# Kernel optimization log

Measured on AMD Instinct MI355X. Metric: run time of the kernel, lower is better.

Reference implementation:

```python
import jax, jax.numpy as jnp
import numpy as np
import math

EMBED_DIM = 1024
NUM_HEADS = 16
QK_DIM = 64
SCALE = 1.0 / math.sqrt(QK_DIM)  # beta=None -> 1/sqrt(qk_dim)


def setup_inputs() -> dict:
    key = jax.random.key(0)
    k1, k2, k3 = jax.random.split(key, 3)
    hidden_states = jax.random.normal(k1, (2, 2048, EMBED_DIM), dtype=jnp.float32)
    # nn.init.normal_(std=0.002)
    query_proj = 0.002 * jax.random.normal(k2, (NUM_HEADS, QK_DIM, EMBED_DIM), dtype=jnp.float32)
    key_proj = 0.002 * jax.random.normal(k3, (NUM_HEADS, QK_DIM, EMBED_DIM), dtype=jnp.float32)
    query_bias = jnp.zeros((QK_DIM,), dtype=jnp.float32)
    key_bias = jnp.zeros((QK_DIM,), dtype=jnp.float32)
    return {
        "hidden_states": hidden_states,
        "query_proj": query_proj,
        "key_proj": key_proj,
        "query_bias": query_bias,
        "key_bias": key_bias,
    }


def reference(hidden_states, query_proj, key_proj, query_bias, key_bias):
    # queries/keys: [b, n, h, q]
    queries = jnp.einsum("bnd,hqd->bnhq", hidden_states, query_proj) + query_bias
    keys = jnp.einsum("bnd,hqd->bnhq", hidden_states, key_proj) + key_bias
    # scores: [b, h, n, m]
    scores = jnp.einsum("bnhq,bmhq->bhnm", queries, keys)
    # energy: -sum logsumexp over last dim, divided by scale
    lse = jax.scipy.special.logsumexp(SCALE * scores, axis=-1)
    return -jnp.sum(lse) / SCALE
```

## Files before the change

kernel.cpp:

```cpp
#include <hip/hip_runtime.h>
#include <hip/hip_bf16.h>
#include <stdint.h>


typedef __bf16 bf16_t;
typedef bf16_t bf16x8 __attribute__((ext_vector_type(8)));
typedef float f32x4 __attribute__((ext_vector_type(4)));
typedef float f32x16 __attribute__((ext_vector_type(16)));

#define MFMA16(a,b,c) __builtin_amdgcn_mfma_f32_16x16x32_bf16(a,b,c,0,0,0)
#define MFMA32(a,b,c) __builtin_amdgcn_mfma_f32_32x32x16_bf16(a,b,c,0,0,0)

static constexpr int SEQ = 2048, BATCH = 2, EMBED = 1024, NH = 16, QKD = 64;
static constexpr int M_TOT = BATCH * SEQ;
static constexpr int N_TOT = 2 * NH * QKD;
static constexpr float C1 = 0.125f * 1.44269504088896340736f;

#define GLL16(g, l) __builtin_amdgcn_global_load_lds(                       \
    (const __attribute__((address_space(1))) void*)(g),                     \
    (__attribute__((address_space(3))) void*)(l), 16, 0, 0)

__global__ __launch_bounds__(256) void cvt_kernel(
    const float* __restrict__ in, bf16_t* __restrict__ out, int n8)
{
    int i = blockIdx.x * 256 + threadIdx.x;
    const int stride = gridDim.x * 256;
    for (; i < n8; i += stride) {
        const f32x4* p = (const f32x4*)(in + (size_t)i * 8);
        f32x4 a = p[0], b = p[1];
        bf16x8 r;
        r[0]=(bf16_t)a[0]; r[1]=(bf16_t)a[1]; r[2]=(bf16_t)a[2]; r[3]=(bf16_t)a[3];
        r[4]=(bf16_t)b[0]; r[5]=(bf16_t)b[1]; r[6]=(bf16_t)b[2]; r[7]=(bf16_t)b[3];
        *(bf16x8*)(out + (size_t)i * 8) = r;
    }
}

__global__ __launch_bounds__(256) void proj_kernel(
    const bf16_t* __restrict__ A, const bf16_t* __restrict__ B,
    const float* __restrict__ qb, const float* __restrict__ kb,
    bf16_t* __restrict__ C)
{
    __shared__ __align__(16) char sA[8192];
    __shared__ __align__(16) char sB[8192];
    const int t = threadIdx.x;
    const int lane = t & 63, wv = t >> 6;
    const int am0 = blockIdx.y * 128, bn0 = blockIdx.x * 128;
    const int wr = wv >> 1, wc = wv & 1;
    const int l15 = lane & 15, g = lane >> 4;

    const int st_r = 16 * wv + (lane >> 2);
    const int st_e = 8 * ((lane & 3) ^ ((lane >> 3) & 3));
    const bf16_t* ga = A + (size_t)(am0 + st_r) * EMBED + st_e;
    const bf16_t* gb = B + (size_t)(bn0 + st_r) * EMBED + st_e;
    char* la = sA + wv * 1024;
    char* lb = sB + wv * 1024;

    f32x4 acc[4][4] = {};
    for (int kk = 0; kk < EMBED; kk += 32) {
        __syncthreads();
        GLL16(ga + kk,                   la);
        GLL16(ga + kk + 64 * EMBED,      la + 4096);
        GLL16(gb + kk,                   lb);
        GLL16(gb + kk + 64 * EMBED,      lb + 4096);
        __syncthreads();

        bf16x8 af[4], bfv[4];
        const int sw = 16 * (g ^ ((l15 >> 1) & 3));
#pragma unroll
        for (int mt = 0; mt < 4; ++mt) {
            int row = wr * 64 + mt * 16 + l15;
            af[mt] = *(const bf16x8*)(sA + row * 64 + sw);
        }
#pragma unroll
        for (int nt = 0; nt < 4; ++nt) {
            int row = wc * 64 + nt * 16 + l15;
            bfv[nt] = *(const bf16x8*)(sB + row * 64 + sw);
        }
#pragma unroll
        for (int mt = 0; mt < 4; ++mt)
#pragma unroll
            for (int nt = 0; nt < 4; ++nt)
                acc[mt][nt] = MFMA16(af[mt], bfv[nt], acc[mt][nt]);
    }

#pragma unroll
    for (int nt = 0; nt < 4; ++nt) {
        int col = bn0 + wc * 64 + nt * 16 + l15;
        float bias, scale;
        if (col < NH * QKD) { bias = qb[col & 63]; scale = C1; }
        else                { bias = kb[col & 63]; scale = 1.0f; }
#pragma unroll
        for (int mt = 0; mt < 4; ++mt)
#pragma unroll
            for (int j = 0; j < 4; ++j) {
                int row = am0 + wr * 64 + mt * 16 + g * 4 + j;
                C[(size_t)row * N_TOT + col] = (bf16_t)((acc[mt][nt][j] + bias) * scale);
            }
    }
}

__global__ __launch_bounds__(256) void lse_kernel(
    const bf16_t* __restrict__ qk, float* __restrict__ partials)
{
    __shared__ __align__(16) char sK[32768];
    const int t = threadIdx.x, lane = t & 63, wv = t >> 6;
    const int pair = blockIdx.y, b = pair >> 4, h = pair & 15;
    const int qr0 = blockIdx.x * 128;
    const int l31 = lane & 31, g5 = lane >> 5;
    const size_t base = (size_t)b * SEQ;

    bf16x8 qf[4];
    const bf16_t* qptr = qk + (base + qr0 + wv * 32 + l31) * N_TOT + h * QKD + g5 * 8;
#pragma unroll
    for (int kf = 0; kf < 4; ++kf) qf[kf] = *(const bf16x8*)(qptr + kf * 16);

    const int st_r = wv * 8 + (lane >> 3);
    const int st_e = 8 * ((lane & 7) ^ ((lane >> 3) & 7));
    const bf16_t* kptr = qk + (base + st_r) * N_TOT + NH * QKD + h * QKD + st_e;
    char* ldst = sK + wv * 1024;

    float sume[16];
#pragma unroll
    for (int j = 0; j < 16; ++j) sume[j] = 0.f;

    for (int kc = 0; kc < SEQ; kc += 256) {
        __syncthreads();
#pragma unroll
        for (int is = 0; is < 8; ++is)
            GLL16(kptr + (size_t)(kc + 32 * is) * N_TOT, ldst + is * 4096);
        __syncthreads();

#pragma unroll
        for (int ct = 0; ct < 8; ++ct) {
            f32x16 s = {};
            const int row = ct * 32 + l31;
#pragma unroll
            for (int kf = 0; kf < 4; ++kf) {
                bf16x8 kv = *(const bf16x8*)(sK + row * 128 + 16 * ((2 * kf + g5) ^ (lane & 7)));
                s = MFMA32(qf[kf], kv, s);
            }
#pragma unroll
            for (int j = 0; j < 16; ++j)
                sume[j] += __builtin_amdgcn_exp2f(s[j]);
        }
    }

#pragma unroll
    for (int j = 0; j < 16; ++j) {
#pragma unroll
        for (int m = 1; m < 32; m <<= 1)
            sume[j] += __shfl_xor(sume[j], m);
    }
    float tt = 0.f;
#pragma unroll
    for (int j = 0; j < 16; ++j) tt += __builtin_amdgcn_logf(sume[j]);
    tt += __shfl_xor(tt, 32);

    __shared__ float wsum[4];
    if (lane == 0) wsum[wv] = tt;
    __syncthreads();
    if (t == 0)
        partials[blockIdx.y * gridDim.x + blockIdx.x] = wsum[0] + wsum[1] + wsum[2] + wsum[3];
}

__global__ __launch_bounds__(256) void final_kernel(
    const float* __restrict__ partials, int n, float* __restrict__ out)
{
    float s = 0.f;
    for (int i = threadIdx.x; i < n; i += 256) s += partials[i];
#pragma unroll
    for (int m = 1; m < 64; m <<= 1) s += __shfl_xor(s, m);
    __shared__ float ws[4];
    const int wave = threadIdx.x >> 6, lane = threadIdx.x & 63;
    if (lane == 0) ws[wave] = s;
    __syncthreads();
    if (threadIdx.x == 0)
        out[0] = -8.0f * 0.69314718055994530942f * (ws[0] + ws[1] + ws[2] + ws[3]);
}

extern "C" void kernel_launch(void* const* d_in, const int* in_sizes, int n_in,
                              void* d_out, int out_size, void* d_ws, size_t ws_size,
                              hipStream_t stream)
{
    const float* hs = (const float*)d_in[0];
    const float* qp = (const float*)d_in[1];
    const float* kp = (const float*)d_in[2];
    const float* qb = (const float*)d_in[3];
    const float* kb = (const float*)d_in[4];

    bf16_t* hsb   = (bf16_t*)d_ws;
    bf16_t* projb = hsb + (size_t)M_TOT * EMBED;
    bf16_t* qkb   = projb + (size_t)N_TOT * EMBED;
    float*  partials = (float*)(qkb + (size_t)M_TOT * N_TOT);
    float*  out = (float*)d_out;

    cvt_kernel<<<2048, 256, 0, stream>>>(hs, hsb, M_TOT * EMBED / 8);
    cvt_kernel<<<512, 256, 0, stream>>>(qp, projb, NH * QKD * EMBED / 8);
    cvt_kernel<<<512, 256, 0, stream>>>(kp, projb + (size_t)NH * QKD * EMBED,
                                        NH * QKD * EMBED / 8);
    proj_kernel<<<dim3(N_TOT / 128, M_TOT / 128), 256, 0, stream>>>(
        hsb, projb, qb, kb, qkb);
    lse_kernel<<<dim3(SEQ / 128, BATCH * NH), 256, 0, stream>>>(qkb, partials);
    final_kernel<<<1, 256, 0, stream>>>(partials, (BATCH * NH) * (SEQ / 128), out);
}
```

Before: 71.44 us.

## Fuse conversions, double-buffer projection GEMM, restructure LSE with register-streamed keys

Merges the three fp32-to-bf16 conversion launches into one kernel. The projection GEMM now uses a 64-wide K step with double-buffered LDS prefetch and one barrier per step, and its block IDs are remapped so that neighbouring tiles land on the same XCD. The LSE kernel drops the LDS staging of keys: each wave streams its own 512-key slice straight from global memory into registers with one-step prefetch, holds all 128 query rows, and combines the per-row sums across waves through LDS. These changes aim to cut launch overhead, hide load latency and remove LDS traffic and barriers, at the cost of higher register pressure and uncoalesced global key loads.

```diff
diff --git a/kernel.cpp b/kernel.cpp
--- a/kernel.cpp
+++ b/kernel.cpp
@@ -10,29 +10,33 @@
 
 #define MFMA16(a,b,c) __builtin_amdgcn_mfma_f32_16x16x32_bf16(a,b,c,0,0,0)
 #define MFMA32(a,b,c) __builtin_amdgcn_mfma_f32_32x32x16_bf16(a,b,c,0,0,0)
+#define GLL16(g, l) __builtin_amdgcn_global_load_lds(                       \
+    (const __attribute__((address_space(1))) void*)(g),                     \
+    (__attribute__((address_space(3))) void*)(l), 16, 0, 0)
 
 static constexpr int SEQ = 2048, BATCH = 2, EMBED = 1024, NH = 16, QKD = 64;
 static constexpr int M_TOT = BATCH * SEQ;
 static constexpr int N_TOT = 2 * NH * QKD;
 static constexpr float C1 = 0.125f * 1.44269504088896340736f;
 
-#define GLL16(g, l) __builtin_amdgcn_global_load_lds(                       \
-    (const __attribute__((address_space(1))) void*)(g),                     \
-    (__attribute__((address_space(3))) void*)(l), 16, 0, 0)
-
 __global__ __launch_bounds__(256) void cvt_kernel(
-    const float* __restrict__ in, bf16_t* __restrict__ out, int n8)
+    const float* __restrict__ hs, const float* __restrict__ qp,
+    const float* __restrict__ kp, bf16_t* __restrict__ hsb,
+    bf16_t* __restrict__ projb)
 {
     int i = blockIdx.x * 256 + threadIdx.x;
-    const int stride = gridDim.x * 256;
-    for (; i < n8; i += stride) {
-        const f32x4* p = (const f32x4*)(in + (size_t)i * 8);
-        f32x4 a = p[0], b = p[1];
-        bf16x8 r;
-        r[0]=(bf16_t)a[0]; r[1]=(bf16_t)a[1]; r[2]=(bf16_t)a[2]; r[3]=(bf16_t)a[3];
-        r[4]=(bf16_t)b[0]; r[5]=(bf16_t)b[1]; r[6]=(bf16_t)b[2]; r[7]=(bf16_t)b[3];
-        *(bf16x8*)(out + (size_t)i * 8) = r;
-    }
+    const float* src; bf16_t* dst;
+    if (i < 524288) { src = hs + (size_t)i * 8; dst = hsb + (size_t)i * 8; }
+    else {
+        int j = i - 524288;
+        dst = projb + (size_t)j * 8;
+        src = (j < 131072) ? qp + (size_t)j * 8 : kp + (size_t)(j - 131072) * 8;
+    }
+    f32x4 a = ((const f32x4*)src)[0], b = ((const f32x4*)src)[1];
+    bf16x8 r;
+    r[0]=(bf16_t)a[0]; r[1]=(bf16_t)a[1]; r[2]=(bf16_t)a[2]; r[3]=(bf16_t)a[3];
+    r[4]=(bf16_t)b[0]; r[5]=(bf16_t)b[1]; r[6]=(bf16_t)b[2]; r[7]=(bf16_t)b[3];
+    *(bf16x8*)dst = r;
 }
 
 __global__ __launch_bounds__(256) void proj_kernel(
@@ -40,47 +44,61 @@
     const float* __restrict__ qb, const float* __restrict__ kb,
     bf16_t* __restrict__ C)
 {
-    __shared__ __align__(16) char sA[8192];
-    __shared__ __align__(16) char sB[8192];
-    const int t = threadIdx.x;
-    const int lane = t & 63, wv = t >> 6;
-    const int am0 = blockIdx.y * 128, bn0 = blockIdx.x * 128;
+    __shared__ __align__(16) char sA[2][16384];
+    __shared__ __align__(16) char sB[2][16384];
+    const int t = threadIdx.x, lane = t & 63, wv = t >> 6;
+    const int bid = blockIdx.x;
+    const int xcd = bid & 7, idx = bid >> 3;
+    const int am0 = (xcd * 4 + (idx >> 4)) * 128;
+    const int bn0 = (idx & 15) * 128;
     const int wr = wv >> 1, wc = wv & 1;
     const int l15 = lane & 15, g = lane >> 4;
 
-    const int st_r = 16 * wv + (lane >> 2);
-    const int st_e = 8 * ((lane & 3) ^ ((lane >> 3) & 3));
-    const bf16_t* ga = A + (size_t)(am0 + st_r) * EMBED + st_e;
-    const bf16_t* gb = B + (size_t)(bn0 + st_r) * EMBED + st_e;
-    char* la = sA + wv * 1024;
-    char* lb = sB + wv * 1024;
+    const int srow = wv * 8 + (lane >> 3);
+    const int sgr  = (lane & 7) ^ ((lane >> 3) & 7);
+    const bf16_t* ga = A + (size_t)(am0 + srow) * EMBED + sgr * 8;
+    const bf16_t* gb = B + (size_t)(bn0 + srow) * EMBED + sgr * 8;
+    const int lbase = wv * 1024;
 
     f32x4 acc[4][4] = {};
-    for (int kk = 0; kk < EMBED; kk += 32) {
+
+#pragma unroll
+    for (int is = 0; is < 4; ++is) {
+        GLL16(ga + (size_t)is * 32 * EMBED, &sA[0][lbase + is * 4096]);
+        GLL16(gb + (size_t)is * 32 * EMBED, &sB[0][lbase + is * 4096]);
+    }
+    __syncthreads();
+
+    int cur = 0;
+    for (int kk = 0; kk < EMBED; kk += 64) {
+        if (kk + 64 < EMBED) {
+#pragma unroll
+            for (int is = 0; is < 4; ++is) {
+                GLL16(ga + kk + 64 + (size_t)is * 32 * EMBED, &sA[cur ^ 1][lbase + is * 4096]);
+                GLL16(gb + kk + 64 + (size_t)is * 32 * EMBED, &sB[cur ^ 1][lbase + is * 4096]);
+            }
+        }
+#pragma unroll
+        for (int s = 0; s < 2; ++s) {
+            bf16x8 af[4], bfv[4];
+#pragma unroll
+            for (int mt = 0; mt < 4; ++mt) {
+                int row = wr * 64 + mt * 16 + l15;
+                af[mt] = *(const bf16x8*)&sA[cur][row * 128 + 16 * (((s << 2) | g) ^ (row & 7))];
+            }
+#pragma unroll
+            for (int nt = 0; nt < 4; ++nt) {
+                int row = wc * 64 + nt * 16 + l15;
+                bfv[nt] = *(const bf16x8*)&sB[cur][row * 128 + 16 * (((s << 2) | g) ^ (row & 7))];
+            }
+#pragma unroll
+            for (int mt = 0; mt < 4; ++mt)
+#pragma unroll
+                for (int nt = 0; nt < 4; ++nt)
+                    acc[mt][nt] = MFMA16(af[mt], bfv[nt], acc[mt][nt]);
+        }
         __syncthreads();
-        GLL16(ga + kk,                   la);
-        GLL16(ga + kk + 64 * EMBED,      la + 4096);
-        GLL16(gb + kk,                   lb);
-        GLL16(gb + kk + 64 * EMBED,      lb + 4096);
-        __syncthreads();
-
-        bf16x8 af[4], bfv[4];
-        const int sw = 16 * (g ^ ((l15 >> 1) & 3));
-#pragma unroll
-        for (int mt = 0; mt < 4; ++mt) {
-            int row = wr * 64 + mt * 16 + l15;
-            af[mt] = *(const bf16x8*)(sA + row * 64 + sw);
-        }
-#pragma unroll
-        for (int nt = 0; nt < 4; ++nt) {
-            int row = wc * 64 + nt * 16 + l15;
-            bfv[nt] = *(const bf16x8*)(sB + row * 64 + sw);
-        }
-#pragma unroll
-        for (int mt = 0; mt < 4; ++mt)
-#pragma unroll
-            for (int nt = 0; nt < 4; ++nt)
-                acc[mt][nt] = MFMA16(af[mt], bfv[nt], acc[mt][nt]);
+        cur ^= 1;
     }
 
 #pragma unroll
@@ -102,65 +120,80 @@
 __global__ __launch_bounds__(256) void lse_kernel(
     const bf16_t* __restrict__ qk, float* __restrict__ partials)
 {
-    __shared__ __align__(16) char sK[32768];
+    __shared__ float rows_s[4][128];
+    __shared__ float ws[4];
     const int t = threadIdx.x, lane = t & 63, wv = t >> 6;
-    const int pair = blockIdx.y, b = pair >> 4, h = pair & 15;
-    const int qr0 = blockIdx.x * 128;
+    const int bid = blockIdx.x;
+    const int xcd = bid & 7, idx = bid >> 3;
+    const int pair = xcd * 4 + (idx >> 4);
+    const int tile = idx & 15;
+    const int b = pair >> 4, h = pair & 15;
+    const int qr0 = tile * 128;
     const int l31 = lane & 31, g5 = lane >> 5;
     const size_t base = (size_t)b * SEQ;
 
-    bf16x8 qf[4];
-    const bf16_t* qptr = qk + (base + qr0 + wv * 32 + l31) * N_TOT + h * QKD + g5 * 8;
-#pragma unroll
-    for (int kf = 0; kf < 4; ++kf) qf[kf] = *(const bf16x8*)(qptr + kf * 16);
-
-    const int st_r = wv * 8 + (lane >> 3);
-    const int st_e = 8 * ((lane & 7) ^ ((lane >> 3) & 7));
-    const bf16_t* kptr = qk + (base + st_r) * N_TOT + NH * QKD + h * QKD + st_e;
-    char* ldst = sK + wv * 1024;
-
-    float sume[16];
-#pragma unroll
-    for (int j = 0; j < 16; ++j) sume[j] = 0.f;
-
-    for (int kc = 0; kc < SEQ; kc += 256) {
-        __syncthreads();
-#pragma unroll
-        for (int is = 0; is < 8; ++is)
-            GLL16(kptr + (size_t)(kc + 32 * is) * N_TOT, ldst + is * 4096);
-        __syncthreads();
-
-#pragma unroll
-        for (int ct = 0; ct < 8; ++ct) {
-            f32x16 s = {};
-            const int row = ct * 32 + l31;
-#pragma unroll
-            for (int kf = 0; kf < 4; ++kf) {
-                bf16x8 kv = *(const bf16x8*)(sK + row * 128 + 16 * ((2 * kf + g5) ^ (lane & 7)));
-                s = MFMA32(qf[kf], kv, s);
-            }
+    bf16x8 qf[4][4];
+#pragma unroll
+    for (int mt = 0; mt < 4; ++mt) {
+        const bf16_t* qp_ = qk + (base + qr0 + mt * 32 + l31) * N_TOT + h * QKD + g5 * 8;
+#pragma unroll
+        for (int kf = 0; kf < 4; ++kf)
+            qf[mt][kf] = *(const bf16x8*)(qp_ + kf * 16);
+    }
+
+    const bf16_t* kb_ = qk + (base + wv * 512 + l31) * N_TOT + NH * QKD + h * QKD + g5 * 8;
+
+    float sume[4] = {0.f, 0.f, 0.f, 0.f};
+
+    bf16x8 kv[4];
+#pragma unroll
+    for (int kf = 0; kf < 4; ++kf) kv[kf] = *(const bf16x8*)(kb_ + kf * 16);
+
+    for (int ct = 0; ct < 16; ++ct) {
+        bf16x8 kn[4];
+        const bf16_t* kn_p = kb_ + (size_t)((ct < 15 ? ct + 1 : 15) * 32) * N_TOT;
+#pragma unroll
+        for (int kf = 0; kf < 4; ++kf) kn[kf] = *(const bf16x8*)(kn_p + kf * 16);
+
+        f32x16 sacc[4];
+#pragma unroll
+        for (int mt = 0; mt < 4; ++mt) {
+            f32x16 z = {};
+            sacc[mt] = z;
+#pragma unroll
+            for (int kf = 0; kf < 4; ++kf)
+                sacc[mt] = MFMA32(kv[kf], qf[mt][kf], sacc[mt]);
+        }
+#pragma unroll
+        for (int mt = 0; mt < 4; ++mt) {
+            float e = 0.f;
 #pragma unroll
             for (int j = 0; j < 16; ++j)
-                sume[j] += __builtin_amdgcn_exp2f(s[j]);
-        }
-    }
-
-#pragma unroll
-    for (int j = 0; j < 16; ++j) {
-#pragma unroll
-        for (int m = 1; m < 32; m <<= 1)
-            sume[j] += __shfl_xor(sume[j], m);
-    }
-    float tt = 0.f;
-#pragma unroll
-    for (int j = 0; j < 16; ++j) tt += __builtin_amdgcn_logf(sume[j]);
-    tt += __shfl_xor(tt, 32);
-
-    __shared__ float wsum[4];
-    if (lane == 0) wsum[wv] = tt;
+                e += __builtin_amdgcn_exp2f(sacc[mt][j]);
+            sume[mt] += e;
+        }
+#pragma unroll
+        for (int kf = 0; kf < 4; ++kf) kv[kf] = kn[kf];
+    }
+
+#pragma unroll
+    for (int mt = 0; mt < 4; ++mt) {
+        float v = sume[mt] + __shfl_xor(sume[mt], 32);
+        if (g5 == 0) rows_s[wv][mt * 32 + l31] = v;
+    }
+    __syncthreads();
+
+    float lg = 0.f;
+    if (t < 128) {
+        float tot = rows_s[0][t] + rows_s[1][t] + rows_s[2][t] + rows_s[3][t];
+        lg = __builtin_amdgcn_logf(tot);
+    }
+#pragma unroll
+    for (int m = 1; m < 64; m <<= 1) lg += __shfl_xor(lg, m);
+    if (lane == 0) ws[wv] = lg;
     __syncthreads();
     if (t == 0)
-        partials[blockIdx.y * gridDim.x + blockIdx.x] = wsum[0] + wsum[1] + wsum[2] + wsum[3];
+        partials[bid] = ws[0] + ws[1] + ws[2] + ws[3];
 }
 
 __global__ __launch_bounds__(256) void final_kernel(
@@ -170,12 +203,12 @@
     for (int i = threadIdx.x; i < n; i += 256) s += partials[i];
 #pragma unroll
     for (int m = 1; m < 64; m <<= 1) s += __shfl_xor(s, m);
-    __shared__ float ws[4];
+    __shared__ float wsf[4];
     const int wave = threadIdx.x >> 6, lane = threadIdx.x & 63;
-    if (lane == 0) ws[wave] = s;
+    if (lane == 0) wsf[wave] = s;
     __syncthreads();
     if (threadIdx.x == 0)
-        out[0] = -8.0f * 0.69314718055994530942f * (ws[0] + ws[1] + ws[2] + ws[3]);
+        out[0] = -8.0f * 0.69314718055994530942f * (wsf[0] + wsf[1] + wsf[2] + wsf[3]);
 }
 
 extern "C" void kernel_launch(void* const* d_in, const int* in_sizes, int n_in,
@@ -194,12 +227,8 @@
     float*  partials = (float*)(qkb + (size_t)M_TOT * N_TOT);
     float*  out = (float*)d_out;
 
-    cvt_kernel<<<2048, 256, 0, stream>>>(hs, hsb, M_TOT * EMBED / 8);
-    cvt_kernel<<<512, 256, 0, stream>>>(qp, projb, NH * QKD * EMBED / 8);
-    cvt_kernel<<<512, 256, 0, stream>>>(kp, projb + (size_t)NH * QKD * EMBED,
-                                        NH * QKD * EMBED / 8);
-    proj_kernel<<<dim3(N_TOT / 128, M_TOT / 128), 256, 0, stream>>>(
-        hsb, projb, qb, kb, qkb);
-    lse_kernel<<<dim3(SEQ / 128, BATCH * NH), 256, 0, stream>>>(qkb, partials);
-    final_kernel<<<1, 256, 0, stream>>>(partials, (BATCH * NH) * (SEQ / 128), out);
-}
+    cvt_kernel<<<3072, 256, 0, stream>>>(hs, qp, kp, hsb, projb);
+    proj_kernel<<<512, 256, 0, stream>>>(hsb, projb, qb, kb, qkb);
+    lse_kernel<<<512, 256, 0, stream>>>(qkb, partials);
+    final_kernel<<<1, 256, 0, stream>>>(partials, 512, out);
+}
```

New measurement: 58.71 us. 17.8% less time.
